# Kernel tuning notes

Hardware: AMD Instinct MI355X
Metric: run time of the kernel (lower is better)

The kernel has to match this reference:

```python
import jax, jax.numpy as jnp
import numpy as np

LN_EPS = 1e-5


def setup_inputs() -> dict:
    key = jax.random.key(0)
    ks = jax.random.split(key, 4)
    B, N, E, H = 2, 512, 128, 256
    h = jax.random.normal(ks[0], (B, N, E), dtype=jnp.float32)
    gamma = jnp.ones((E,), dtype=jnp.float32)
    beta = jnp.zeros((E,), dtype=jnp.float32)
    # First Linear: in_dim = 2E, out_dim = H. Stored as [2E, H] (x @ W1 + b1).
    W1 = jax.random.normal(ks[1], (2 * E, H), dtype=jnp.float32) / np.sqrt(2 * E)
    b1 = jnp.zeros((H,), dtype=jnp.float32)
    # Second Linear: [H, 1] squeezed to [H], scalar bias.
    w2 = jax.random.normal(ks[2], (H,), dtype=jnp.float32) / np.sqrt(H)
    b2 = jnp.zeros((), dtype=jnp.float32)
    return {"h": h, "gamma": gamma, "beta": beta, "W1": W1, "b1": b1,
            "w2": w2, "b2": b2}


def reference(h, gamma, beta, W1, b1, w2, b2):
    # LayerNorm over E
    mu = jnp.mean(h, axis=-1, keepdims=True)
    var = jnp.mean(jnp.square(h - mu), axis=-1, keepdims=True)
    h_n = (h - mu) * jax.lax.rsqrt(var + LN_EPS) * gamma + beta  # [B,N,E]

    E = h_n.shape[-1]
    # Decompose Linear(concat(h_i, h_j)) = h_i @ Wa + h_j @ Wb + b1
    Wa, Wb = W1[:E], W1[E:]
    a = jnp.einsum('bne,eh->bnh', h_n, Wa)  # contribution of first slot
    b = jnp.einsum('bne,eh->bnh', h_n, Wb)  # contribution of second slot
    # Pairwise pre-activation for the (i,j) ordering: [B,N,N,H]
    z_ij = a[:, :, None, :] + b[:, None, :, :] + b1
    g = jax.nn.gelu(z_ij, approximate=False)  # torch GELU is exact (erf)
    l_ij = jnp.einsum('bijh,h->bij', g, w2) + b2  # [B,N,N]
    # l_ji[b,i,j] == l_ij[b,j,i], so reuse via transpose (same math as
    # running the MLP twice on swapped concat order).
    return 0.5 * (l_ij + jnp.swapaxes(l_ij, 1, 2))
```

## Files before the change

### kernel.cpp

```cpp
#include <hip/hip_runtime.h>
#include <math.h>

#define EDIM 128
#define HDIM 256
#define NDIM 512
#define BDIM 2
#define LN_EPS 1e-5f

__global__ __launch_bounds__(256) void k_ln_proj(
    const float* __restrict__ hptr, const float* __restrict__ gamma,
    const float* __restrict__ beta, const float* __restrict__ W1,
    const float* __restrict__ b1, float* __restrict__ a_out,
    float* __restrict__ b_out)
{
    __shared__ float hn_s[4][EDIM];
    const int tid = threadIdx.x;
    const int r = tid >> 6;
    const int lane = tid & 63;
    const int row0 = blockIdx.x * 4;
    const float2 v = *(const float2*)(hptr + (row0 + r) * EDIM + lane * 2);
    float s  = v.x + v.y;
    float ss = v.x * v.x + v.y * v.y;
    #pragma unroll
    for (int k = 32; k >= 1; k >>= 1) {
        s  += __shfl_xor(s, k, 64);
        ss += __shfl_xor(ss, k, 64);
    }
    const float mu  = s * (1.0f / EDIM);
    const float var = ss * (1.0f / EDIM) - mu * mu;
    const float rs  = rsqrtf(var + LN_EPS);
    const float2 g2 = *(const float2*)(gamma + lane * 2);
    const float2 be = *(const float2*)(beta + lane * 2);
    hn_s[r][lane * 2]     = (v.x - mu) * rs * g2.x + be.x;
    hn_s[r][lane * 2 + 1] = (v.y - mu) * rs * g2.y + be.y;
    __syncthreads();
    float sa0 = 0.f, sa1 = 0.f, sa2 = 0.f, sa3 = 0.f;
    float sb0 = 0.f, sb1 = 0.f, sb2 = 0.f, sb3 = 0.f;
    #pragma unroll 4
    for (int e = 0; e < EDIM; ++e) {
        const float wa = W1[e * HDIM + tid];
        const float wb = W1[(EDIM + e) * HDIM + tid];
        const float h0 = hn_s[0][e], h1 = hn_s[1][e];
        const float h2 = hn_s[2][e], h3 = hn_s[3][e];
        sa0 = fmaf(h0, wa, sa0); sa1 = fmaf(h1, wa, sa1);
        sa2 = fmaf(h2, wa, sa2); sa3 = fmaf(h3, wa, sa3);
        sb0 = fmaf(h0, wb, sb0); sb1 = fmaf(h1, wb, sb1);
        sb2 = fmaf(h2, wb, sb2); sb3 = fmaf(h3, wb, sb3);
    }
    const float bb1 = b1[tid];
    a_out[(row0 + 0) * HDIM + tid] = sa0;
    a_out[(row0 + 1) * HDIM + tid] = sa1;
    a_out[(row0 + 2) * HDIM + tid] = sa2;
    a_out[(row0 + 3) * HDIM + tid] = sa3;
    b_out[(row0 + 0) * HDIM + tid] = sb0 + bb1;
    b_out[(row0 + 1) * HDIM + tid] = sb1 + bb1;
    b_out[(row0 + 2) * HDIM + tid] = sb2 + bb1;
    b_out[(row0 + 3) * HDIM + tid] = sb3 + bb1;
}

__device__ __forceinline__ float gelu_fast(float z) {
    const float z2 = z * z;
    const float q  = fmaf(-0.10294826f, z2, -2.3022082f);
    const float e  = __builtin_amdgcn_exp2f(z * q);
    const float r  = __builtin_amdgcn_rcpf(1.0f + e);
    return z * r;
}

#define HHALF 128
#define PAD 132

__global__ __launch_bounds__(256) void k_pair(
    const float* __restrict__ a, const float* __restrict__ bpb,
    const float* __restrict__ w2, const float* __restrict__ b2,
    float* __restrict__ out)
{
    __shared__ float a_s[32][PAD];
    __shared__ float b_s[32][PAD];
    __shared__ float w2_s[HDIM];
    const int blk = blockIdx.x;
    const int bb = blk >> 8;
    const int bi = (blk >> 4) & 15;
    const int bj = blk & 15;
    const int tid = threadIdx.x;

    const float* arow = a + (bb * NDIM + bi * 32) * HDIM;
    const float* brow = bpb + (bb * NDIM + bj * 32) * HDIM;

    if (tid < HDIM / 4) ((float4*)w2_s)[tid] = ((const float4*)w2)[tid];

    const int ti = tid >> 4, tj = tid & 15;
    const float* ap0 = a_s[ti];
    const float* ap1 = a_s[ti + 16];
    const float* bp0 = b_s[tj];
    const float* bp1 = b_s[tj + 16];
    float acc00 = 0.f, acc01 = 0.f, acc10 = 0.f, acc11 = 0.f;

    #pragma unroll
    for (int half = 0; half < 2; ++half) {
        if (half) __syncthreads();
        const float* ar = arow + half * HHALF;
        const float* br = brow + half * HHALF;
        #pragma unroll
        for (int idx = tid; idx < 32 * (HHALF / 4); idx += 256) {
            const int r = idx >> 5;
            const int c = idx & 31;
            *(float4*)&a_s[r][c * 4] = *(const float4*)(ar + r * HDIM + c * 4);
            *(float4*)&b_s[r][c * 4] = *(const float4*)(br + r * HDIM + c * 4);
        }
        __syncthreads();
        const float* wp = w2_s + half * HHALF;
        #pragma unroll 4
        for (int hh = 0; hh < HHALF; hh += 4) {
            const float4 a0  = *(const float4*)(ap0 + hh);
            const float4 a1  = *(const float4*)(ap1 + hh);
            const float4 b0  = *(const float4*)(bp0 + hh);
            const float4 b1v = *(const float4*)(bp1 + hh);
            const float4 wv  = *(const float4*)(wp + hh);
            acc00 = fmaf(wv.x, gelu_fast(a0.x + b0.x),  acc00);
            acc01 = fmaf(wv.x, gelu_fast(a0.x + b1v.x), acc01);
            acc10 = fmaf(wv.x, gelu_fast(a1.x + b0.x),  acc10);
            acc11 = fmaf(wv.x, gelu_fast(a1.x + b1v.x), acc11);
            acc00 = fmaf(wv.y, gelu_fast(a0.y + b0.y),  acc00);
            acc01 = fmaf(wv.y, gelu_fast(a0.y + b1v.y), acc01);
            acc10 = fmaf(wv.y, gelu_fast(a1.y + b0.y),  acc10);
            acc11 = fmaf(wv.y, gelu_fast(a1.y + b1v.y), acc11);
            acc00 = fmaf(wv.z, gelu_fast(a0.z + b0.z),  acc00);
            acc01 = fmaf(wv.z, gelu_fast(a0.z + b1v.z), acc01);
            acc10 = fmaf(wv.z, gelu_fast(a1.z + b0.z),  acc10);
            acc11 = fmaf(wv.z, gelu_fast(a1.z + b1v.z), acc11);
            acc00 = fmaf(wv.w, gelu_fast(a0.w + b0.w),  acc00);
            acc01 = fmaf(wv.w, gelu_fast(a0.w + b1v.w), acc01);
            acc10 = fmaf(wv.w, gelu_fast(a1.w + b0.w),  acc10);
            acc11 = fmaf(wv.w, gelu_fast(a1.w + b1v.w), acc11);
        }
    }
    const float bias = b2[0];
    const int i0 = bi * 32 + ti;
    const int j0 = bj * 32 + tj;
    float* ob = out + (bb * NDIM + i0) * NDIM;
    ob[j0]      = acc00 + bias;
    ob[j0 + 16] = acc01 + bias;
    ob += 16 * NDIM;
    ob[j0]      = acc10 + bias;
    ob[j0 + 16] = acc11 + bias;
}

__global__ __launch_bounds__(256) void k_sym(float* __restrict__ out) {
    __shared__ float Ta[32][33];
    __shared__ float Tb[32][33];
    const int blk = blockIdx.x;
    const int b  = blk >> 8;
    const int ti = (blk >> 4) & 15;
    const int tj = blk & 15;
    if (tj < ti) return;
    float* base = out + b * NDIM * NDIM;
    const int tx = threadIdx.x & 31;
    const int ty = threadIdx.x >> 5;
    #pragma unroll
    for (int r = ty; r < 32; r += 8) {
        Ta[r][tx] = base[(ti * 32 + r) * NDIM + tj * 32 + tx];
        Tb[r][tx] = base[(tj * 32 + r) * NDIM + ti * 32 + tx];
    }
    __syncthreads();
    #pragma unroll
    for (int r = ty; r < 32; r += 8) {
        base[(ti * 32 + r) * NDIM + tj * 32 + tx] = 0.5f * (Ta[r][tx] + Tb[tx][r]);
    }
    if (ti != tj) {
        #pragma unroll
        for (int r = ty; r < 32; r += 8) {
            base[(tj * 32 + r) * NDIM + ti * 32 + tx] = 0.5f * (Tb[r][tx] + Ta[tx][r]);
        }
    }
}

extern "C" void kernel_launch(void* const* d_in, const int* in_sizes, int n_in,
                              void* d_out, int out_size, void* d_ws, size_t ws_size,
                              hipStream_t stream) {
    const float* hptr  = (const float*)d_in[0];
    const float* gamma = (const float*)d_in[1];
    const float* beta  = (const float*)d_in[2];
    const float* W1    = (const float*)d_in[3];
    const float* b1    = (const float*)d_in[4];
    const float* w2    = (const float*)d_in[5];
    const float* b2    = (const float*)d_in[6];
    float* out = (float*)d_out;

    float* a_ws = (float*)d_ws;
    float* b_ws = a_ws + BDIM * NDIM * HDIM;

    k_ln_proj<<<(BDIM * NDIM) / 4, 256, 0, stream>>>(hptr, gamma, beta, W1, b1, a_ws, b_ws);
    k_pair<<<BDIM * 256, 256, 0, stream>>>(a_ws, b_ws, w2, b2, out);
    k_sym<<<BDIM * 256, 256, 0, stream>>>(out);
}
```

Baseline: 57.70 us.

## Pack GELU math into float2 vectors and halve pair-kernel j-tile

Rewrites the GELU evaluation in the pairwise kernel to operate on two-wide float vectors, so the compiler can emit packed FP32 instructions (v_pk_fma/v_pk_mul) for the polynomial, add and accumulate steps; exp2 and rcp remain scalar. Each thread now computes two output elements instead of four, and the j tile shrinks from 32 to 16 rows, doubling the grid to 1024 blocks for better CU fill. In exchange, each block reloads the a-tile more often relative to its compute, and per-thread reuse of loaded a/b values is lower.

```diff
diff --git a/kernel.cpp b/kernel.cpp
--- a/kernel.cpp
+++ b/kernel.cpp
@@ -6,6 +6,8 @@
 #define NDIM 512
 #define BDIM 2
 #define LN_EPS 1e-5f
+
+typedef float v2f __attribute__((ext_vector_type(2)));
 
 __global__ __launch_bounds__(256) void k_ln_proj(
     const float* __restrict__ hptr, const float* __restrict__ gamma,
@@ -58,11 +60,19 @@
     b_out[(row0 + 3) * HDIM + tid] = sb3 + bb1;
 }
 
-__device__ __forceinline__ float gelu_fast(float z) {
-    const float z2 = z * z;
-    const float q  = fmaf(-0.10294826f, z2, -2.3022082f);
-    const float e  = __builtin_amdgcn_exp2f(z * q);
-    const float r  = __builtin_amdgcn_rcpf(1.0f + e);
+__device__ __forceinline__ v2f gelu2(v2f z) {
+    const v2f c2 = {-0.10294826f, -0.10294826f};
+    const v2f c1 = {-2.3022082f, -2.3022082f};
+    const v2f z2 = z * z;
+    const v2f q  = __builtin_elementwise_fma(c2, z2, c1);
+    const v2f p  = z * q;
+    v2f e;
+    e.x = __builtin_amdgcn_exp2f(p.x);
+    e.y = __builtin_amdgcn_exp2f(p.y);
+    const v2f d = e + 1.0f;
+    v2f r;
+    r.x = __builtin_amdgcn_rcpf(d.x);
+    r.y = __builtin_amdgcn_rcpf(d.y);
     return z * r;
 }
 
@@ -75,74 +85,65 @@
     float* __restrict__ out)
 {
     __shared__ float a_s[32][PAD];
-    __shared__ float b_s[32][PAD];
+    __shared__ float b_s[16][PAD];
     __shared__ float w2_s[HDIM];
     const int blk = blockIdx.x;
-    const int bb = blk >> 8;
-    const int bi = (blk >> 4) & 15;
-    const int bj = blk & 15;
+    const int bb = blk >> 9;
+    const int bi = (blk >> 5) & 15;
+    const int bj = blk & 31;
     const int tid = threadIdx.x;
 
     const float* arow = a + (bb * NDIM + bi * 32) * HDIM;
-    const float* brow = bpb + (bb * NDIM + bj * 32) * HDIM;
+    const float* brow = bpb + (bb * NDIM + bj * 16) * HDIM;
 
     if (tid < HDIM / 4) ((float4*)w2_s)[tid] = ((const float4*)w2)[tid];
 
     const int ti = tid >> 4, tj = tid & 15;
     const float* ap0 = a_s[ti];
     const float* ap1 = a_s[ti + 16];
-    const float* bp0 = b_s[tj];
-    const float* bp1 = b_s[tj + 16];
-    float acc00 = 0.f, acc01 = 0.f, acc10 = 0.f, acc11 = 0.f;
+    const float* bp  = b_s[tj];
+    v2f acc0 = {0.f, 0.f}, acc1 = {0.f, 0.f};
 
     #pragma unroll
     for (int half = 0; half < 2; ++half) {
         if (half) __syncthreads();
-        const float* ar = arow + half * HHALF;
-        const float* br = brow + half * HHALF;
         #pragma unroll
-        for (int idx = tid; idx < 32 * (HHALF / 4); idx += 256) {
-            const int r = idx >> 5;
-            const int c = idx & 31;
-            *(float4*)&a_s[r][c * 4] = *(const float4*)(ar + r * HDIM + c * 4);
-            *(float4*)&b_s[r][c * 4] = *(const float4*)(br + r * HDIM + c * 4);
+        for (int idx = tid; idx < 1536; idx += 256) {
+            if (idx < 1024) {
+                const int r = idx >> 5, c = idx & 31;
+                *(float4*)&a_s[r][c * 4] =
+                    *(const float4*)(arow + r * HDIM + half * HHALF + c * 4);
+            } else {
+                const int k = idx - 1024;
+                const int r = k >> 5, c = k & 31;
+                *(float4*)&b_s[r][c * 4] =
+                    *(const float4*)(brow + r * HDIM + half * HHALF + c * 4);
+            }
         }
         __syncthreads();
         const float* wp = w2_s + half * HHALF;
         #pragma unroll 4
         for (int hh = 0; hh < HHALF; hh += 4) {
-            const float4 a0  = *(const float4*)(ap0 + hh);
-            const float4 a1  = *(const float4*)(ap1 + hh);
-            const float4 b0  = *(const float4*)(bp0 + hh);
-            const float4 b1v = *(const float4*)(bp1 + hh);
-            const float4 wv  = *(const float4*)(wp + hh);
-            acc00 = fmaf(wv.x, gelu_fast(a0.x + b0.x),  acc00);
-            acc01 = fmaf(wv.x, gelu_fast(a0.x + b1v.x), acc01);
-            acc10 = fmaf(wv.x, gelu_fast(a1.x + b0.x),  acc10);
-            acc11 = fmaf(wv.x, gelu_fast(a1.x + b1v.x), acc11);
-            acc00 = fmaf(wv.y, gelu_fast(a0.y + b0.y),  acc00);
-            acc01 = fmaf(wv.y, gelu_fast(a0.y + b1v.y), acc01);
-            acc10 = fmaf(wv.y, gelu_fast(a1.y + b0.y),  acc10);
-            acc11 = fmaf(wv.y, gelu_fast(a1.y + b1v.y), acc11);
-            acc00 = fmaf(wv.z, gelu_fast(a0.z + b0.z),  acc00);
-            acc01 = fmaf(wv.z, gelu_fast(a0.z + b1v.z), acc01);
-            acc10 = fmaf(wv.z, gelu_fast(a1.z + b0.z),  acc10);
-            acc11 = fmaf(wv.z, gelu_fast(a1.z + b1v.z), acc11);
-            acc00 = fmaf(wv.w, gelu_fast(a0.w + b0.w),  acc00);
-            acc01 = fmaf(wv.w, gelu_fast(a0.w + b1v.w), acc01);
-            acc10 = fmaf(wv.w, gelu_fast(a1.w + b0.w),  acc10);
-            acc11 = fmaf(wv.w, gelu_fast(a1.w + b1v.w), acc11);
+            const float4 a0 = *(const float4*)(ap0 + hh);
+            const float4 a1 = *(const float4*)(ap1 + hh);
+            const float4 b0 = *(const float4*)(bp + hh);
+            const float4 wv = *(const float4*)(wp + hh);
+            const v2f alo0 = {a0.x, a0.y}, ahi0 = {a0.z, a0.w};
+            const v2f alo1 = {a1.x, a1.y}, ahi1 = {a1.z, a1.w};
+            const v2f blo  = {b0.x, b0.y}, bhi  = {b0.z, b0.w};
+            const v2f wlo  = {wv.x, wv.y}, whi  = {wv.z, wv.w};
+            acc0 = __builtin_elementwise_fma(wlo, gelu2(alo0 + blo), acc0);
+            acc0 = __builtin_elementwise_fma(whi, gelu2(ahi0 + bhi), acc0);
+            acc1 = __builtin_elementwise_fma(wlo, gelu2(alo1 + blo), acc1);
+            acc1 = __builtin_elementwise_fma(whi, gelu2(ahi1 + bhi), acc1);
         }
     }
     const float bias = b2[0];
     const int i0 = bi * 32 + ti;
-    const int j0 = bj * 32 + tj;
-    float* ob = out + (bb * NDIM + i0) * NDIM;
-    ob[j0]      = acc00 + bias;
-    ob[j0 + 16] = acc01 + bias;
-    ob += 16 * NDIM;
-    ob[j0]      = acc10 + bias;
-    ob[j0 + 16] = acc11 + bias;
+    const int j0 = bj * 16 + tj;
+    float* ob = out + (bb * NDIM + i0) * NDIM + j0;
+    ob[0]         = acc0.x + acc0.y + bias;
+    ob[16 * NDIM] = acc1.x + acc1.y + bias;
 }
 
 __global__ __launch_bounds__(256) void k_sym(float* __restrict__ out) {
@@ -190,6 +191,6 @@
     float* b_ws = a_ws + BDIM * NDIM * HDIM;
 
     k_ln_proj<<<(BDIM * NDIM) / 4, 256, 0, stream>>>(hptr, gamma, beta, W1, b1, a_ws, b_ws);
-    k_pair<<<BDIM * 256, 256, 0, stream>>>(a_ws, b_ws, w2, b2, out);
+    k_pair<<<BDIM * 512, 256, 0, stream>>>(a_ws, b_ws, w2, b2, out);
     k_sym<<<BDIM * 256, 256, 0, stream>>>(out);
 }
```

Measured after the change: 49.23 us. 1.17x faster.
